# Optimization experiments

Hardware: AMD Instinct MI355X
Metric: run time of the kernel (lower is better)

## Reference

```python
import jax, jax.numpy as jnp
import numpy as np

B, T, HID = 2, 2048, 2048
NKH, NVH = 16, 32
DK, DV = 128, 128
R = NVH // NKH            # GQA repeat factor = 2
KDIM, VDIM = NKH * DK, NVH * DV   # 2048, 4096
CONV_K = 4
EPS = 1e-6


def _silu(x):
    return x * jax.nn.sigmoid(x)


def _l2norm(x, eps=1e-6):
    return x * jax.lax.rsqrt(jnp.sum(x * x, axis=-1, keepdims=True) + eps)


def setup_inputs() -> dict:
    key = jax.random.key(0)
    ks = jax.random.split(key, 8)
    w = lambda k, shape, sc=0.02: jax.random.normal(k, shape, jnp.float32) * sc
    return {
        "hidden_states": jax.random.normal(ks[0], (B, T, HID), jnp.float32),
        "W_qkvz": w(ks[1], (HID, 2 * KDIM + 2 * VDIM)),
        "W_ba": w(ks[2], (HID, 2 * NVH)),
        "conv_w": w(ks[3], (2 * KDIM + VDIM, CONV_K), 0.1),
        "dt_bias": jnp.ones((NVH,), jnp.float32),
        "A_log": jax.random.normal(ks[4], (NVH,), jnp.float32),
        "norm_weight": jnp.ones((DV,), jnp.float32),
        "W_out": w(ks[5], (VDIM, HID)),
    }


def reference(hidden_states, W_qkvz, W_ba, conv_w, dt_bias, A_log, norm_weight, W_out):
    Bv, Tv = hidden_states.shape[:2]
    # input projections
    qkvz = hidden_states @ W_qkvz              # [B,T,2*KDIM+2*VDIM]
    ba = hidden_states @ W_ba                  # [B,T,2*NVH]
    # fix_query_key_value_ordering: per k-head layout [dk, dk, R*dv, R*dv]
    qkvz = qkvz.reshape(Bv, Tv, NKH, 2 * DK + 2 * R * DV)
    q, k, v, z = jnp.split(qkvz, [DK, 2 * DK, 2 * DK + R * DV], axis=3)
    v = v.reshape(Bv, Tv, NVH, DV)
    z = z.reshape(Bv, Tv, NVH, DV)
    ba = ba.reshape(Bv, Tv, NKH, 2 * R)
    b, a = jnp.split(ba, 2, axis=3)
    b = b.reshape(Bv, Tv, NVH)
    a = a.reshape(Bv, Tv, NVH)
    # causal depthwise short conv over time + silu
    mixed = jnp.concatenate(
        [q.reshape(Bv, Tv, KDIM), k.reshape(Bv, Tv, KDIM), v.reshape(Bv, Tv, VDIM)], axis=-1)
    xp = jnp.pad(mixed, ((0, 0), (CONV_K - 1, 0), (0, 0)))
    conv = sum(xp[:, j:j + Tv, :] * conv_w[:, j] for j in range(CONV_K))
    conv = _silu(conv)
    q, k, v = jnp.split(conv, [KDIM, 2 * KDIM], axis=-1)
    q = q.reshape(Bv, Tv, NKH, DK)
    k = k.reshape(Bv, Tv, NKH, DK)
    v = v.reshape(Bv, Tv, NVH, DV)
    # gates
    beta = jax.nn.sigmoid(b)                                   # [B,T,H]
    g = -jnp.exp(A_log) * jax.nn.softplus(a + dt_bias)         # [B,T,H] log-decay
    alpha = jnp.exp(g)
    # GQA expansion + fused qk l2norm + scale
    q = jnp.repeat(q, R, axis=2)
    k = jnp.repeat(k, R, axis=2)
    q = _l2norm(q) * (DK ** -0.5)
    k = _l2norm(k)
    # gated delta rule recurrence over time; state S: [B,H,dk,dv]
    def step(S, inp):
        q_t, k_t, v_t, a_t, b_t = inp
        S = S * a_t[..., None, None]
        err = jnp.einsum('bhkv,bhk->bhv', S, k_t)
        v_new = (v_t - err) * b_t[..., None]
        S = S + k_t[..., None] * v_new[..., None, :]
        o = jnp.einsum('bhkv,bhk->bhv', S, q_t)
        return S, o

    tm = lambda x: jnp.swapaxes(x, 0, 1)  # time-major
    S0 = jnp.zeros((Bv, NVH, DK, DV), hidden_states.dtype)
    _, o = jax.lax.scan(step, S0, (tm(q), tm(k), tm(v), tm(alpha), tm(beta)))
    o = jnp.swapaxes(o, 0, 1)             # [B,T,H,DV]
    # gated RMSNorm (Mamba2 style: gate before norm)
    og = o * _silu(z)
    og = og * jax.lax.rsqrt(jnp.mean(og * og, axis=-1, keepdims=True) + EPS) * norm_weight
    return og.reshape(Bv, Tv, VDIM) @ W_out
```

## Files before the change

kernel.cpp:

```cpp
#include <hip/hip_runtime.h>
#include <hip/hip_bf16.h>

typedef __hip_bfloat16 bf16;
typedef __bf16 bf16x8_t __attribute__((ext_vector_type(8)));
typedef float f32x4 __attribute__((ext_vector_type(4)));
typedef unsigned short u16;

#define TB 2
#define TT 2048
#define THID 2048
#define TNKH 16
#define TNVH 32
#define TDK 128
#define TDV 128
#define TKDIM 2048
#define TVDIM 4096
#define CCH 64
#define NCH 32

__device__ __forceinline__ unsigned short f2bu(float f) {
  __hip_bfloat16 h = __float2bfloat16(f);
  return *reinterpret_cast<unsigned short*>(&h);
}
__device__ __forceinline__ float bu2f(unsigned short u) {
  __hip_bfloat16 h;
  *reinterpret_cast<unsigned short*>(&h) = u;
  return __bfloat162float(h);
}

__device__ __forceinline__ void gl_lds16(const bf16* g, u16* l) {
  __builtin_amdgcn_global_load_lds(
      (const __attribute__((address_space(1))) unsigned int*)g,
      (__attribute__((address_space(3))) unsigned int*)l, 16, 0, 0);
}

__global__ __launch_bounds__(256) void init_small_kernel(
    const void* __restrict__ dtb_raw, const void* __restrict__ alog_raw,
    const void* __restrict__ nw_raw,
    bf16* __restrict__ dtb_b, bf16* __restrict__ alog_b, bf16* __restrict__ nw_b,
    unsigned* __restrict__ flag)
{
  const unsigned* du = (const unsigned*)dtb_raw;
  const bool isb = (du[0] == 0x3F803F80u);
  const int t = threadIdx.x;
  if (t == 0) flag[0] = isb ? 1u : 0u;
  if (isb) {
    if (t < 32)       ((u16*)dtb_b)[t]       = ((const u16*)dtb_raw)[t];
    else if (t < 64)  ((u16*)alog_b)[t - 32] = ((const u16*)alog_raw)[t - 32];
    else if (t < 192) ((u16*)nw_b)[t - 64]   = ((const u16*)nw_raw)[t - 64];
  } else {
    if (t < 32)       dtb_b[t]        = __float2bfloat16(((const float*)dtb_raw)[t]);
    else if (t < 64)  alog_b[t - 32]  = __float2bfloat16(((const float*)alog_raw)[t - 32]);
    else if (t < 192) nw_b[t - 64]    = __float2bfloat16(((const float*)nw_raw)[t - 64]);
  }
}

__global__ __launch_bounds__(256) void convert_kernel(
    const void* __restrict__ src, bf16* __restrict__ dst, int n,
    const unsigned* __restrict__ dtb, int skipb) {
  const bool isb = (dtb[0] == 0x3F803F80u);
  if (isb && skipb) return;
  int i = blockIdx.x * 256 + threadIdx.x;
  const int stride = gridDim.x * 256;
  if (isb) {
    const unsigned short* s = (const unsigned short*)src;
    unsigned short* d = (unsigned short*)dst;
    for (; i < n; i += stride) d[i] = s[i];
  } else {
    const float* s = (const float*)src;
    for (; i < n; i += stride) dst[i] = __float2bfloat16(s[i]);
  }
}

__global__ __launch_bounds__(256) void transpose_convert_kernel(
    const void* __restrict__ src, bf16* __restrict__ dst, int K, int N,
    const unsigned* __restrict__ dtb) {
  __shared__ unsigned short tile[32][33];
  const bool isb = (dtb[0] == 0x3F803F80u);
  const int n0 = blockIdx.x * 32, k0 = blockIdx.y * 32;
  const int tx = threadIdx.x & 31, ty = threadIdx.x >> 5;
#pragma unroll
  for (int i = 0; i < 4; i++) {
    const int k = k0 + ty + i * 8;
    unsigned short v;
    if (isb) v = ((const unsigned short*)src)[(size_t)k * N + n0 + tx];
    else     v = f2bu(((const float*)src)[(size_t)k * N + n0 + tx]);
    tile[ty + i * 8][tx] = v;
  }
  __syncthreads();
#pragma unroll
  for (int i = 0; i < 4; i++) {
    const int n = n0 + ty + i * 8;
    ((unsigned short*)dst)[(size_t)n * K + k0 + tx] = tile[tx][ty + i * 8];
  }
}

#define PH_PRE()  do {                                                        \
    asm volatile("s_waitcnt lgkmcnt(0)" ::: "memory");                        \
    __builtin_amdgcn_sched_barrier(0); } while (0)
#define PH_POST() do { __builtin_amdgcn_sched_barrier(0);                     \
    __builtin_amdgcn_s_barrier(); } while (0)

#define STAGE_A(buf, kt, s)                                                   \
  gl_lds16(&Ak[(size_t)(m0 + (s) * 64 + srow) * lda + (kt) * 64 + scol],      \
           &lds[buf][0][((s) * 8192 + wave * 1024) >> 1])
#define STAGE_B(buf, kt, s)                                                   \
  gl_lds16(&Btk[(size_t)(n0 + (s) * 64 + srow) * ldb + (kt) * 64 + scol],     \
           &lds[buf][1][((s) * 8192 + wave * 1024) >> 1])

#define READ_A(buf, mh)                                                       \
  do {                                                                        \
    _Pragma("unroll")                                                         \
    for (int mi2 = 0; mi2 < 4; mi2++) {                                       \
      const int row_ = wm * 128 + (mh) * 64 + mi2 * 16 + l16;                 \
      aF[mi2][0] = *reinterpret_cast<const bf16x8_t*>(                        \
          &lds[buf][0][(row_ * 128 + koff0) >> 1]);                           \
      aF[mi2][1] = *reinterpret_cast<const bf16x8_t*>(                        \
          &lds[buf][0][(row_ * 128 + koff1) >> 1]);                           \
    }                                                                         \
  } while (0)

#define READ_B(buf, nh)                                                       \
  do {                                                                        \
    _Pragma("unroll")                                                         \
    for (int ni2 = 0; ni2 < 2; ni2++) {                                       \
      const int row_ = wn * 64 + ((nh) * 2 + ni2) * 16 + l16;                 \
      bF[(nh) * 2 + ni2][0] = *reinterpret_cast<const bf16x8_t*>(             \
          &lds[buf][1][(row_ * 128 + koff0) >> 1]);                           \
      bF[(nh) * 2 + ni2][1] = *reinterpret_cast<const bf16x8_t*>(             \
          &lds[buf][1][(row_ * 128 + koff1) >> 1]);                           \
    }                                                                         \
  } while (0)

#define MMA_Q(mh, nh)                                                         \
  do {                                                                        \
    __builtin_amdgcn_s_setprio(1);                                            \
    _Pragma("unroll")                                                         \
    for (int ks = 0; ks < 2; ks++)                                            \
      _Pragma("unroll")                                                       \
      for (int mi2 = 0; mi2 < 4; mi2++)                                       \
        _Pragma("unroll")                                                     \
        for (int ni2 = 0; ni2 < 2; ni2++)                                     \
          acc[(mh) * 4 + mi2][(nh) * 2 + ni2] =                               \
              __builtin_amdgcn_mfma_f32_16x16x32_bf16(                        \
                  aF[mi2][ks], bF[(nh) * 2 + ni2][ks],                        \
                  acc[(mh) * 4 + mi2][(nh) * 2 + ni2], 0, 0, 0);              \
    __builtin_amdgcn_s_setprio(0);                                            \
  } while (0)

template<int MODE>
__global__ __launch_bounds__(512, 2) void gemm256_kernel(
    const bf16* __restrict__ A, const bf16* __restrict__ Bt,
    void* __restrict__ C0, bf16* __restrict__ C1,
    int M, int N, int K, int lda, int ldb,
    const unsigned* __restrict__ flag, const void* __restrict__ Araw)
{
  __shared__ __align__(16) u16 lds[2][2][256 * 64];

  const int tid = threadIdx.x;
  const int wave = tid >> 6, lane = tid & 63;
  const int l16 = lane & 15, quad = lane >> 4;
  const int wm = wave >> 2, wn = wave & 3;

  const int nwg = gridDim.x * gridDim.y;
  const int lin = blockIdx.y * gridDim.x + blockIdx.x;
  const int cpx = nwg >> 3;
  const int sw = (lin & 7) * cpx + (lin >> 3);
  const int m0 = (sw / gridDim.x) * 256;
  const int n0 = (sw % gridDim.x) * 256;

  const bf16* Abase = A;
  if (MODE == 1 && Araw != nullptr && flag[0] != 0u)
    Abase = (const bf16*)Araw;

  const bf16* Ak  = Abase + (size_t)blockIdx.z * K;
  const bf16* Btk = Bt + (size_t)blockIdx.z * K;

  f32x4 acc[8][4];
#pragma unroll
  for (int i = 0; i < 8; i++)
#pragma unroll
    for (int j = 0; j < 4; j++) acc[i][j] = (f32x4){0.f, 0.f, 0.f, 0.f};

  const int o_lane = wave * 1024 + lane * 16;
  const int l_lane = o_lane ^ ((lane & 56) << 1);
  const int srow = l_lane >> 7;
  const int scol = (l_lane & 127) >> 1;
  const int koff0 = (quad * 16) ^ ((l16 & 7) << 4);
  const int koff1 = koff0 ^ 64;

  bf16x8_t aF[4][2], bF[4][2];

  const int NT = K >> 6;
  const int NIT = NT >> 1;

#pragma unroll
  for (int s = 0; s < 4; s++) STAGE_B(0, 0, s);
#pragma unroll
  for (int s = 0; s < 4; s++) STAGE_A(0, 0, s);
#pragma unroll
  for (int s = 0; s < 4; s++) STAGE_B(1, 1, s);
  asm volatile("s_waitcnt vmcnt(4)" ::: "memory");
  __builtin_amdgcn_s_barrier();

  for (int it = 0; it < NIT; ++it) {
    const int to = 2 * it + 1, te2 = 2 * it + 2, to2 = 2 * it + 3;
    const bool s2 = (te2 < NT), s3 = (to2 < NT);

    STAGE_A(1, to, 0); STAGE_A(1, to, 1);
    READ_A(0, 0); READ_B(0, 0);
    PH_PRE(); MMA_Q(0, 0); PH_POST();

    STAGE_A(1, to, 2); STAGE_A(1, to, 3);
    READ_B(0, 1);
    PH_PRE(); MMA_Q(0, 1); PH_POST();

    if (s2) { STAGE_B(0, te2, 0); STAGE_B(0, te2, 1); }
    READ_A(0, 1);
    PH_PRE(); MMA_Q(1, 1); PH_POST();

    if (s2) { STAGE_B(0, te2, 2); STAGE_B(0, te2, 3); }
    PH_PRE(); MMA_Q(1, 0);
    if (s2) asm volatile("s_waitcnt vmcnt(4)" ::: "memory");
    else    asm volatile("s_waitcnt vmcnt(0)" ::: "memory");
    PH_POST();

    if (s2) { STAGE_A(0, te2, 0); STAGE_A(0, te2, 1); }
    READ_A(1, 0); READ_B(1, 0);
    PH_PRE(); MMA_Q(0, 0); PH_POST();

    if (s2) { STAGE_A(0, te2, 2); STAGE_A(0, te2, 3); }
    READ_B(1, 1);
    PH_PRE(); MMA_Q(0, 1); PH_POST();

    if (s3) { STAGE_B(1, to2, 0); STAGE_B(1, to2, 1); }
    READ_A(1, 1);
    PH_PRE(); MMA_Q(1, 1); PH_POST();

    if (s3) { STAGE_B(1, to2, 2); STAGE_B(1, to2, 3); }
    PH_PRE(); MMA_Q(1, 0);
    if (s2) {
      if (s3) asm volatile("s_waitcnt vmcnt(4)" ::: "memory");
      else    asm volatile("s_waitcnt vmcnt(0)" ::: "memory");
    }
    PH_POST();
  }

#pragma unroll
  for (int mi = 0; mi < 8; mi++)
#pragma unroll
    for (int ni = 0; ni < 4; ni++)
#pragma unroll
      for (int r = 0; r < 4; r++) {
        const int row = m0 + wm * 128 + mi * 16 + quad * 4 + r;
        const int col = n0 + wn * 64 + ni * 16 + l16;
        const float fv = acc[mi][ni][r];
        if (MODE == 2) {
          float* Cp = (float*)C0 + (size_t)blockIdx.z * 4096 * 2048;
          Cp[(size_t)row * N + col] = fv;
        } else {
          const bf16 v = __float2bfloat16(fv);
          bf16* C0h = (bf16*)C0;
          const int hh = col / 768;
          const int idx = col - hh * 768;
          if (idx < 128) {
            C0h[(size_t)row * 8192 + hh * 128 + idx] = v;
          } else if (idx < 256) {
            C0h[(size_t)row * 8192 + 2048 + hh * 128 + (idx - 128)] = v;
          } else if (idx < 512) {
            const int u = idx - 256;
            C0h[(size_t)row * 8192 + 4096 + (hh * 2 + (u >> 7)) * 128 + (u & 127)] = v;
          } else {
            const int u = idx - 512;
            C1[(size_t)row * 4096 + (hh * 2 + (u >> 7)) * 128 + (u & 127)] = v;
          }
        }
      }
}

__global__ __launch_bounds__(256) void combine_kernel(
    const float* __restrict__ p, void* __restrict__ out,
    const unsigned* __restrict__ flag)
{
  const bool outbf = (flag[0] != 0u);
  const size_t i = ((size_t)blockIdx.x * 256 + threadIdx.x) * 4;
  const float4 a = *reinterpret_cast<const float4*>(&p[i]);
  const float4 b = *reinterpret_cast<const float4*>(&p[i + (size_t)4096 * 2048]);
  if (outbf) {
    unsigned short o[4];
    o[0] = f2bu(a.x + b.x); o[1] = f2bu(a.y + b.y);
    o[2] = f2bu(a.z + b.z); o[3] = f2bu(a.w + b.w);
    *reinterpret_cast<uint2*>((unsigned short*)out + i) =
        *reinterpret_cast<const uint2*>(o);
  } else {
    float4 s;
    s.x = a.x + b.x; s.y = a.y + b.y; s.z = a.z + b.z; s.w = a.w + b.w;
    *reinterpret_cast<float4*>((float*)out + i) = s;
  }
}

__global__ __launch_bounds__(256) void ba_gates_kernel(
    const bf16* __restrict__ hs, const void* __restrict__ hs_raw,
    const bf16* __restrict__ W_ba,
    const bf16* __restrict__ dt_bias, const bf16* __restrict__ A_log,
    float* __restrict__ gb, float* __restrict__ beta,
    const unsigned* __restrict__ flag)
{
  const int m = blockIdx.x * 4 + (threadIdx.x >> 6);
  const int c = threadIdx.x & 63;
  const bf16* hbase = (flag[0] != 0u) ? (const bf16*)hs_raw : hs;
  const bf16* hrow = hbase + (size_t)m * THID;
  float acc = 0.f;
  for (int k = 0; k < THID; k += 8) {
    const uint4 hv = *reinterpret_cast<const uint4*>(&hrow[k]);
    const unsigned short* hp = (const unsigned short*)&hv;
#pragma unroll
    for (int j = 0; j < 8; j++)
      acc += bu2f(hp[j]) * __bfloat162float(W_ba[(size_t)(k + j) * 64 + c]);
  }
  const int h = c >> 2, q = c & 3;
  if (q < 2) {
    beta[(size_t)m * TNVH + h * 2 + q] = 1.f / (1.f + __expf(-acc));
  } else {
    const int vh = h * 2 + (q - 2);
    const float av = acc + __bfloat162float(dt_bias[vh]);
    const float sp = (av > 20.f) ? av : log1pf(__expf(av));
    gb[(size_t)m * TNVH + vh] = -__expf(__bfloat162float(A_log[vh])) * sp;
  }
}

#define CTM 8
__global__ __launch_bounds__(128) void conv_kernel(
    const bf16* __restrict__ mixed, const bf16* __restrict__ conv_w,
    bf16* __restrict__ qn, bf16* __restrict__ kn, bf16* __restrict__ vc)
{
  __shared__ float red[CTM][2];
  const int g = blockIdx.x;
  const int m0 = blockIdx.y * CTM;
  const int tloc = m0 & (TT - 1);
  const int tid = threadIdx.x;
  const int c = g * 128 + tid;

  float w[4];
#pragma unroll
  for (int j = 0; j < 4; j++) w[j] = __bfloat162float(conv_w[c * 4 + j]);

  float xv[CTM + 3];
#pragma unroll
  for (int jj = 0; jj < CTM + 3; jj++) {
    const int row = m0 - 3 + jj;
    xv[jj] = (row >= 0) ? bu2f(((const unsigned short*)mixed)[(size_t)row * 8192 + c]) : 0.f;
  }

  float val[CTM];
#pragma unroll
  for (int u = 0; u < CTM; u++) {
    float s = 0.f;
#pragma unroll
    for (int j = 0; j < 4; j++) {
      if (tloc + u - 3 + j >= 0) s += xv[u + j] * w[j];
    }
    val[u] = s / (1.f + __expf(-s));
  }

  if (g < 32) {
#pragma unroll
    for (int u = 0; u < CTM; u++) {
      float s2 = val[u] * val[u];
#pragma unroll
      for (int off = 32; off; off >>= 1) s2 += __shfl_xor(s2, off);
      if ((tid & 63) == 0) red[u][tid >> 6] = s2;
    }
    __syncthreads();
#pragma unroll
    for (int u = 0; u < CTM; u++) {
      float scale = rsqrtf(red[u][0] + red[u][1] + 1e-6f);
      const int m = m0 + u;
      if (g < 16) {
        scale *= 0.08838834764831845f;
        qn[(size_t)m * TKDIM + g * 128 + tid] = __float2bfloat16(val[u] * scale);
      } else {
        kn[(size_t)m * TKDIM + (g - 16) * 128 + tid] = __float2bfloat16(val[u] * scale);
      }
    }
  } else {
#pragma unroll
    for (int u = 0; u < CTM; u++)
      vc[(size_t)(m0 + u) * TVDIM + (g - 32) * 128 + tid] = __float2bfloat16(val[u]);
  }
}

__global__ __launch_bounds__(256) void chunk_prep_kernel(
    const bf16* __restrict__ qn, const bf16* __restrict__ kn,
    const bf16* __restrict__ vc, const float* __restrict__ gb,
    const float* __restrict__ betab,
    bf16* __restrict__ Wbuf, bf16* __restrict__ U0buf,
    bf16* __restrict__ Pbuf, bf16* __restrict__ Ktt,
    float* __restrict__ egcbuf)
{
  __shared__ __align__(16) unsigned short Kb[64][136];
  __shared__ __align__(16) unsigned short Vb[64][136];
  __shared__ __align__(8) float Ms[64][66];
  __shared__ float gcl[64], bl[64], egl[64], ecl[64];

  const int cg = blockIdx.x;
  const int vh = blockIdx.y;
  const int h = vh >> 1;
  const int ch = cg * 32 + vh;
  const int m0 = cg * 64;
  const int tid = threadIdx.x;
  const int lane = tid & 63;
  const int w = tid >> 6, l16 = lane & 15, quad = lane >> 4;

  {
    const int row = tid >> 2, cb = (tid & 3) * 32;
#pragma unroll
    for (int u = 0; u < 4; u++) {
      *reinterpret_cast<uint4*>(&Kb[row][cb + u * 8]) =
          *reinterpret_cast<const uint4*>(&kn[(size_t)(m0 + row) * TKDIM + h * 128 + cb + u * 8]);
      *reinterpret_cast<uint4*>(&Vb[row][cb + u * 8]) =
          *reinterpret_cast<const uint4*>(&vc[(size_t)(m0 + row) * TVDIM + vh * 128 + cb + u * 8]);
    }
  }
  if (tid < 64) {
    float x = gb[(size_t)(m0 + tid) * TNVH + vh];
#pragma unroll
    for (int off = 1; off < 64; off <<= 1) {
      float y = __shfl_up(x, off);
      if (lane >= off) x += y;
    }
    gcl[tid] = x;
    egl[tid] = __expf(x);
    bl[tid] = betab[(size_t)(m0 + tid) * TNVH + vh];
  }
  __syncthreads();

  if (tid < 64) {
    ecl[tid] = __expf(gcl[63] - gcl[tid]);
    egcbuf[(size_t)ch * 64 + tid] = egl[tid];
  }

  f32x4 aKK[4], aQK[4];
#pragma unroll
  for (int i = 0; i < 4; i++) { aKK[i] = (f32x4){0.f,0.f,0.f,0.f}; aQK[i] = (f32x4){0.f,0.f,0.f,0.f}; }
#pragma unroll
  for (int kk = 0; kk < 4; kk++) {
    bf16x8_t kf = *reinterpret_cast<const bf16x8_t*>(&Kb[w * 16 + l16][kk * 32 + quad * 8]);
    bf16x8_t qf = *reinterpret_cast<const bf16x8_t*>(
        &qn[(size_t)(m0 + w * 16 + l16) * TKDIM + h * 128 + kk * 32 + quad * 8]);
#pragma unroll
    for (int nt = 0; nt < 4; nt++) {
      bf16x8_t bf = *reinterpret_cast<const bf16x8_t*>(&Kb[nt * 16 + l16][kk * 32 + quad * 8]);
      aKK[nt] = __builtin_amdgcn_mfma_f32_16x16x32_bf16(kf, bf, aKK[nt], 0, 0, 0);
      aQK[nt] = __builtin_amdgcn_mfma_f32_16x16x32_bf16(qf, bf, aQK[nt], 0, 0, 0);
    }
  }
#pragma unroll
  for (int nt = 0; nt < 4; nt++)
#pragma unroll
    for (int r = 0; r < 4; r++) {
      const int i = w * 16 + quad * 4 + r;
      const int s = nt * 16 + l16;
      const float d = gcl[i] - gcl[s];
      const float e = __expf(d);
      Ms[i][s] = (s < i) ? bl[i] * e * aKK[nt][r] : 0.f;
      const float pv = (s <= i) ? e * aQK[nt][r] : 0.f;
      Pbuf[(size_t)ch * 4096 + i * 64 + s] = __float2bfloat16(pv);
    }
  __syncthreads();

  {
    const int j = tid;
    float x[64];
    if (j < 128) {
#pragma unroll
      for (int i = 0; i < 64; i++) x[i] = bl[i] * egl[i] * bu2f(Kb[i][j]);
    } else {
#pragma unroll
      for (int i = 0; i < 64; i++) x[i] = bl[i] * bu2f(Vb[i][j - 128]);
    }
#pragma unroll
    for (int i = 1; i < 64; i++) {
      float xi = x[i];
#pragma unroll
      for (int s = 0; s < (i & ~1); s += 2) {
        const float2 m2 = *reinterpret_cast<const float2*>(&Ms[i][s]);
        xi -= m2.x * x[s] + m2.y * x[s + 1];
      }
      if (i & 1) xi -= Ms[i][i - 1] * x[i - 1];
      x[i] = xi;
    }
    if (j < 128) {
#pragma unroll
      for (int i = 0; i < 64; i++)
        Wbuf[(size_t)ch * 8192 + i * 128 + j] = __float2bfloat16(x[i]);
    } else {
#pragma unroll
      for (int i = 0; i < 64; i++)
        U0buf[(size_t)ch * 8192 + i * 128 + (j - 128)] = __float2bfloat16(x[i]);
    }
  }

#pragma unroll
  for (int u = 0; u < 32; u++) {
    const int idx = tid + u * 256;
    const int s = idx & 63, k = idx >> 6;
    Ktt[(size_t)ch * 8192 + k * 64 + s] = __float2bfloat16(bu2f(Kb[s][k]) * ecl[s]);
  }
}

__global__ __launch_bounds__(256) void chunk_scan_kernel(
    const bf16* __restrict__ qn, const bf16* __restrict__ zb,
    const float* __restrict__ egcbuf,
    const bf16* __restrict__ Wbuf, const bf16* __restrict__ U0buf,
    const bf16* __restrict__ Pbuf, const bf16* __restrict__ Ktt,
    bf16* __restrict__ ogbuf, float* __restrict__ psum)
{
  __shared__ __align__(16) unsigned short STb[32][136];
  __shared__ __align__(16) unsigned short uT[32][72];

  const int d = blockIdx.x;
  const int jj = d >> 3;
  const int bvh = (d & 7) * 8 + (jj >> 2);
  const int sl = jj & 3;
  const int b = bvh >> 5, vh = bvh & 31, h = vh >> 1;

  const int tid = threadIdx.x;
  const int w = tid >> 6, lane = tid & 63;
  const int l16 = lane & 15, quad = lane >> 4;
  const int vt = w & 1, kh = (w >> 1) * 64;

  for (int idx = tid; idx < 32 * 136; idx += 256) ((unsigned short*)STb)[idx] = 0;

  bf16x8_t wf[4], qf[4];
  unsigned short u0r[2][4];
  {
    const int ch0 = (b * 32) * 32 + vh;
    const int m00 = (b * 32) * 64;
#pragma unroll
    for (int kk = 0; kk < 4; kk++) {
      wf[kk] = *reinterpret_cast<const bf16x8_t*>(
          &Wbuf[(size_t)ch0 * 8192 + (w * 16 + l16) * 128 + kk * 32 + quad * 8]);
      qf[kk] = *reinterpret_cast<const bf16x8_t*>(
          &qn[(size_t)(m00 + w * 16 + l16) * TKDIM + h * 128 + kk * 32 + quad * 8]);
    }
#pragma unroll
    for (int nt = 0; nt < 2; nt++)
#pragma unroll
      for (int r = 0; r < 4; r++) {
        const int i = w * 16 + quad * 4 + r;
        const int dvg = sl * 32 + nt * 16 + l16;
        u0r[nt][r] = ((const unsigned short*)U0buf)[(size_t)ch0 * 8192 + i * 128 + dvg];
      }
  }
  f32x4 STreg[4];
#pragma unroll
  for (int i = 0; i < 4; i++) STreg[i] = (f32x4){0.f, 0.f, 0.f, 0.f};

  asm volatile("s_waitcnt lgkmcnt(0)" ::: "memory");
  __builtin_amdgcn_sched_barrier(0);
  __builtin_amdgcn_s_barrier();

  for (int c = 0; c < NCH; c++) {
    const int ch = (b * 32 + c) * 32 + vh;
    const int m0 = (b * 32 + c) * 64;
    const int cn = (c + 1 < NCH) ? c + 1 : c;
    const int chn = (b * 32 + cn) * 32 + vh;
    const int m0n = (b * 32 + cn) * 64;

    bf16x8_t wfn[4], qfn[4];
#pragma unroll
    for (int kk = 0; kk < 4; kk++) {
      wfn[kk] = *reinterpret_cast<const bf16x8_t*>(
          &Wbuf[(size_t)chn * 8192 + (w * 16 + l16) * 128 + kk * 32 + quad * 8]);
      qfn[kk] = *reinterpret_cast<const bf16x8_t*>(
          &qn[(size_t)(m0n + w * 16 + l16) * TKDIM + h * 128 + kk * 32 + quad * 8]);
    }
    unsigned short u0rn[2][4], zr[2][4];
#pragma unroll
    for (int nt = 0; nt < 2; nt++)
#pragma unroll
      for (int r = 0; r < 4; r++) {
        const int i = w * 16 + quad * 4 + r;
        const int dvg = sl * 32 + nt * 16 + l16;
        u0rn[nt][r] = ((const unsigned short*)U0buf)[(size_t)chn * 8192 + i * 128 + dvg];
        zr[nt][r]  = ((const unsigned short*)zb)[(size_t)(m0 + i) * TVDIM + vh * 128 + dvg];
      }
    bf16x8_t pf[2];
#pragma unroll
    for (int kk = 0; kk < 2; kk++)
      pf[kk] = *reinterpret_cast<const bf16x8_t*>(
          &Pbuf[(size_t)ch * 4096 + (w * 16 + l16) * 64 + kk * 32 + quad * 8]);
    bf16x8_t kttf[4][2];
#pragma unroll
    for (int nt = 0; nt < 4; nt++)
#pragma unroll
      for (int kk = 0; kk < 2; kk++)
        kttf[nt][kk] = *reinterpret_cast<const bf16x8_t*>(
            &Ktt[(size_t)ch * 8192 + (kh + nt * 16 + l16) * 64 + kk * 32 + quad * 8]);
    float egr[4];
#pragma unroll
    for (int r = 0; r < 4; r++)
      egr[r] = egcbuf[(size_t)ch * 64 + w * 16 + quad * 4 + r];
    const float egC = egcbuf[(size_t)ch * 64 + 63];

    f32x4 au[2], aq[2];
#pragma unroll
    for (int i = 0; i < 2; i++) { au[i] = (f32x4){0.f,0.f,0.f,0.f}; aq[i] = (f32x4){0.f,0.f,0.f,0.f}; }
#pragma unroll
    for (int kk = 0; kk < 4; kk++)
#pragma unroll
      for (int nt = 0; nt < 2; nt++) {
        bf16x8_t bfr = *reinterpret_cast<const bf16x8_t*>(
            &STb[nt * 16 + l16][kk * 32 + quad * 8]);
        au[nt] = __builtin_amdgcn_mfma_f32_16x16x32_bf16(wf[kk], bfr, au[nt], 0, 0, 0);
        aq[nt] = __builtin_amdgcn_mfma_f32_16x16x32_bf16(qf[kk], bfr, aq[nt], 0, 0, 0);
      }
#pragma unroll
    for (int nt = 0; nt < 2; nt++)
#pragma unroll
      for (int r = 0; r < 4; r++) {
        const int i = w * 16 + quad * 4 + r;
        uT[nt * 16 + l16][i] = f2bu(bu2f(u0r[nt][r]) - au[nt][r]);
      }
    asm volatile("s_waitcnt lgkmcnt(0)" ::: "memory");
    __builtin_amdgcn_sched_barrier(0);
    __builtin_amdgcn_s_barrier();

    f32x4 ao[2];
#pragma unroll
    for (int i = 0; i < 2; i++) ao[i] = (f32x4){0.f,0.f,0.f,0.f};
#pragma unroll
    for (int kk = 0; kk < 2; kk++)
#pragma unroll
      for (int nt = 0; nt < 2; nt++) {
        bf16x8_t bfr = *reinterpret_cast<const bf16x8_t*>(
            &uT[nt * 16 + l16][kk * 32 + quad * 8]);
        ao[nt] = __builtin_amdgcn_mfma_f32_16x16x32_bf16(pf[kk], bfr, ao[nt], 0, 0, 0);
      }
    float og[2][4];
#pragma unroll
    for (int nt = 0; nt < 2; nt++)
#pragma unroll
      for (int r = 0; r < 4; r++) {
        const float o = egr[r] * aq[nt][r] + ao[nt][r];
        const float zv = bu2f(zr[nt][r]);
        og[nt][r] = o * (zv / (1.f + __expf(-zv)));
      }
#pragma unroll
    for (int r = 0; r < 4; r++) {
      float ss = og[0][r] * og[0][r] + og[1][r] * og[1][r];
      ss += __shfl_xor(ss, 1); ss += __shfl_xor(ss, 2);
      ss += __shfl_xor(ss, 4); ss += __shfl_xor(ss, 8);
      if (l16 == 0)
        psum[(size_t)(m0 + w * 16 + quad * 4 + r) * 128 + vh * 4 + sl] = ss;
    }
#pragma unroll
    for (int nt = 0; nt < 2; nt++)
#pragma unroll
      for (int r = 0; r < 4; r++) {
        const int i = w * 16 + quad * 4 + r;
        const int dvg = sl * 32 + nt * 16 + l16;
        ((unsigned short*)ogbuf)[(size_t)(m0 + i) * TVDIM + vh * 128 + dvg] =
            f2bu(og[nt][r]);
      }

    bf16x8_t uf[2];
#pragma unroll
    for (int kk = 0; kk < 2; kk++)
      uf[kk] = *reinterpret_cast<const bf16x8_t*>(&uT[vt * 16 + l16][kk * 32 + quad * 8]);
    f32x4 as_[4];
#pragma unroll
    for (int i = 0; i < 4; i++) as_[i] = (f32x4){0.f,0.f,0.f,0.f};
#pragma unroll
    for (int nt = 0; nt < 4; nt++)
#pragma unroll
      for (int kk = 0; kk < 2; kk++)
        as_[nt] = __builtin_amdgcn_mfma_f32_16x16x32_bf16(uf[kk], kttf[nt][kk], as_[nt], 0, 0, 0);
#pragma unroll
    for (int nt = 0; nt < 4; nt++)
#pragma unroll
      for (int r = 0; r < 4; r++) {
        const float ns = egC * STreg[nt][r] + as_[nt][r];
        STreg[nt][r] = ns;
        STb[vt * 16 + quad * 4 + r][kh + nt * 16 + l16] = f2bu(ns);
      }

#pragma unroll
    for (int kk = 0; kk < 4; kk++) { wf[kk] = wfn[kk]; qf[kk] = qfn[kk]; }
#pragma unroll
    for (int nt = 0; nt < 2; nt++)
#pragma unroll
      for (int r = 0; r < 4; r++) u0r[nt][r] = u0rn[nt][r];
    asm volatile("s_waitcnt lgkmcnt(0)" ::: "memory");
    __builtin_amdgcn_sched_barrier(0);
    __builtin_amdgcn_s_barrier();
  }
}

__global__ __launch_bounds__(256) void norm_finish_kernel(
    bf16* __restrict__ og, const float* __restrict__ psum,
    const bf16* __restrict__ nw)
{
  const size_t idx = ((size_t)blockIdx.x * 256 + threadIdx.x) * 8;
  const int m = (int)(idx >> 12);
  const int col = (int)(idx & 4095);
  const int vh = col >> 7, dv = col & 127;
  const float* ps = &psum[(size_t)m * 128 + vh * 4];
  const float ms = (ps[0] + ps[1] + ps[2] + ps[3]) * (1.f / 128.f);
  const float sc = rsqrtf(ms + 1e-6f);
  uint4 v = *reinterpret_cast<const uint4*>(&og[idx]);
  uint4 wv = *reinterpret_cast<const uint4*>(&nw[dv]);
  unsigned short* vp = (unsigned short*)&v;
  unsigned short* wp = (unsigned short*)&wv;
  uint4 o;
  unsigned short* op = (unsigned short*)&o;
#pragma unroll
  for (int j = 0; j < 8; j++)
    op[j] = f2bu(bu2f(vp[j]) * sc * bu2f(wp[j]));
  *reinterpret_cast<uint4*>(&og[idx]) = o;
}

extern "C" void kernel_launch(void* const* d_in, const int* in_sizes, int n_in,
                              void* d_out, int out_size, void* d_ws, size_t ws_size,
                              hipStream_t stream) {
  const void* hs_raw   = d_in[0];
  const void* Wq_raw   = d_in[1];
  const void* Wba_raw  = d_in[2];
  const void* cw_raw   = d_in[3];
  const void* dtb_raw  = d_in[4];
  const void* Alog_raw = d_in[5];
  const void* nw_raw   = d_in[6];
  const void* Wout_raw = d_in[7];

  const size_t M = (size_t)TB * TT;
  char* p = (char*)d_ws;
  auto alloc = [&](size_t bytes) { char* r = p; p += (bytes + 255) & ~(size_t)255; return r; };
  unsigned* flag  = (unsigned*)alloc(256);
  bf16* hs_b   = (bf16*)alloc(M * THID * 2);
  bf16* WqT    = (bf16*)alloc((size_t)12288 * THID * 2);
  bf16* Wba_b  = (bf16*)alloc((size_t)THID * 64 * 2);
  bf16* cw_b   = (bf16*)alloc(8192 * 4 * 2);
  bf16* dtb_b  = (bf16*)alloc(64);
  bf16* Alog_b = (bf16*)alloc(64);
  bf16* nw_b   = (bf16*)alloc(256);
  bf16* WoutT  = (bf16*)alloc((size_t)THID * TVDIM * 2);
  bf16*  mixed  = (bf16*) alloc(M * 8192 * 2);
  bf16*  zbuf   = (bf16*) alloc(M * 4096 * 2);
  bf16*  qn     = (bf16*) alloc(M * 2048 * 2);
  bf16*  kn     = (bf16*) alloc(M * 2048 * 2);
  bf16*  vc     = (bf16*) alloc(M * 4096 * 2);
  float* gbuf   = (float*)alloc(M * 32 * 4);
  float* betab  = (float*)alloc(M * 32 * 4);
  float* egcbuf = (float*)alloc((size_t)2048 * 64 * 4);
  float* psum   = (float*)alloc(M * 128 * 4);

  bf16* Wbuf  = WqT;
  bf16* Pbuf  = WqT + (size_t)2048 * 64 * 128;
  bf16* U0buf = mixed;
  bf16* Ktt   = mixed + (size_t)2048 * 64 * 128;
  bf16* ogbuf = vc;
  float* part = (float*)mixed;

  const unsigned* dtb_u = (const unsigned*)dtb_raw;

  init_small_kernel<<<1, 256, 0, stream>>>(
      dtb_raw, Alog_raw, nw_raw, dtb_b, Alog_b, nw_b, flag);
  convert_kernel<<<2048, 256, 0, stream>>>(hs_raw, hs_b, (int)(M * THID), dtb_u, 1);
  transpose_convert_kernel<<<dim3(12288 / 32, 2048 / 32), 256, 0, stream>>>(
      Wq_raw, WqT, 2048, 12288, dtb_u);
  convert_kernel<<<128, 256, 0, stream>>>(Wba_raw, Wba_b, THID * 64, dtb_u, 0);
  convert_kernel<<<32,  256, 0, stream>>>(cw_raw,  cw_b,  8192 * 4,  dtb_u, 0);
  transpose_convert_kernel<<<dim3(2048 / 32, 4096 / 32), 256, 0, stream>>>(
      Wout_raw, WoutT, 4096, 2048, dtb_u);

  gemm256_kernel<1><<<dim3(12288 / 256, 4096 / 256), 512, 0, stream>>>(
      hs_b, WqT, mixed, zbuf, 4096, 12288, 2048, 2048, 2048, flag, hs_raw);
  ba_gates_kernel<<<4096 / 4, 256, 0, stream>>>(
      hs_b, hs_raw, Wba_b, dtb_b, Alog_b, gbuf, betab, flag);
  conv_kernel<<<dim3(64, 4096 / CTM), 128, 0, stream>>>(mixed, cw_b, qn, kn, vc);

  chunk_prep_kernel<<<dim3(64, 32), 256, 0, stream>>>(
      qn, kn, vc, gbuf, betab, Wbuf, U0buf, Pbuf, Ktt, egcbuf);
  chunk_scan_kernel<<<256, 256, 0, stream>>>(
      qn, zbuf, egcbuf, Wbuf, U0buf, Pbuf, Ktt, ogbuf, psum);
  norm_finish_kernel<<<8192, 256, 0, stream>>>(ogbuf, psum, nw_b);

  gemm256_kernel<2><<<dim3(2048 / 256, 4096 / 256, 2), 512, 0, stream>>>(
      ogbuf, WoutT, part, nullptr, 4096, 2048, 2048, 4096, 4096, flag, nullptr);
  combine_kernel<<<8192, 256, 0, stream>>>(part, d_out, flag);
}
```

Baseline: 864.2 us.

## Replace split-K output GEMM with 256x128 tile GEMM writing output directly

The output projection used to run as a split-K GEMM with two K halves, writing fp32 partials that a separate combine kernel summed and converted. It now runs as one full-K GEMM templated on a narrower 128-column N tile, so the grid still has 256 workgroups and the result, bf16 or fp32, is stored straight into the output. This drops the partial-buffer traffic and the extra combine launch, at the cost of a longer K loop per workgroup and a smaller B tile. Separately, the hidden-state convert kernel is launched with fewer blocks.

New measurement: 882.6 us. +2.1%, slower.

```diff
diff --git a/kernel.cpp b/kernel.cpp
--- a/kernel.cpp
+++ b/kernel.cpp
@@ -103,10 +103,10 @@
 
 #define STAGE_A(buf, kt, s)                                                   \
   gl_lds16(&Ak[(size_t)(m0 + (s) * 64 + srow) * lda + (kt) * 64 + scol],      \
-           &lds[buf][0][((s) * 8192 + wave * 1024) >> 1])
+           &lds[buf][((s) * 8192 + wave * 1024) >> 1])
 #define STAGE_B(buf, kt, s)                                                   \
   gl_lds16(&Btk[(size_t)(n0 + (s) * 64 + srow) * ldb + (kt) * 64 + scol],     \
-           &lds[buf][1][((s) * 8192 + wave * 1024) >> 1])
+           &lds[buf][16384 + (((s) * 8192 + wave * 1024) >> 1)])
 
 #define READ_A(buf, mh)                                                       \
   do {                                                                        \
@@ -114,21 +114,21 @@
     for (int mi2 = 0; mi2 < 4; mi2++) {                                       \
       const int row_ = wm * 128 + (mh) * 64 + mi2 * 16 + l16;                 \
       aF[mi2][0] = *reinterpret_cast<const bf16x8_t*>(                        \
-          &lds[buf][0][(row_ * 128 + koff0) >> 1]);                           \
+          &lds[buf][(row_ * 128 + koff0) >> 1]);                              \
       aF[mi2][1] = *reinterpret_cast<const bf16x8_t*>(                        \
-          &lds[buf][0][(row_ * 128 + koff1) >> 1]);                           \
+          &lds[buf][(row_ * 128 + koff1) >> 1]);                              \
     }                                                                         \
   } while (0)
 
 #define READ_B(buf, nh)                                                       \
   do {                                                                        \
     _Pragma("unroll")                                                         \
-    for (int ni2 = 0; ni2 < 2; ni2++) {                                       \
-      const int row_ = wn * 64 + ((nh) * 2 + ni2) * 16 + l16;                 \
-      bF[(nh) * 2 + ni2][0] = *reinterpret_cast<const bf16x8_t*>(             \
-          &lds[buf][1][(row_ * 128 + koff0) >> 1]);                           \
-      bF[(nh) * 2 + ni2][1] = *reinterpret_cast<const bf16x8_t*>(             \
-          &lds[buf][1][(row_ * 128 + koff1) >> 1]);                           \
+    for (int ni2 = 0; ni2 < NH; ni2++) {                                      \
+      const int row_ = wn * (NF * 16) + ((nh) * NH + ni2) * 16 + l16;         \
+      bF[(nh) * NH + ni2][0] = *reinterpret_cast<const bf16x8_t*>(            \
+          &lds[buf][16384 + ((row_ * 128 + koff0) >> 1)]);                    \
+      bF[(nh) * NH + ni2][1] = *reinterpret_cast<const bf16x8_t*>(            \
+          &lds[buf][16384 + ((row_ * 128 + koff1) >> 1)]);                    \
     }                                                                         \
   } while (0)
 
@@ -140,22 +140,30 @@
       _Pragma("unroll")                                                       \
       for (int mi2 = 0; mi2 < 4; mi2++)                                       \
         _Pragma("unroll")                                                     \
-        for (int ni2 = 0; ni2 < 2; ni2++)                                     \
-          acc[(mh) * 4 + mi2][(nh) * 2 + ni2] =                               \
+        for (int ni2 = 0; ni2 < NH; ni2++)                                    \
+          acc[(mh) * 4 + mi2][(nh) * NH + ni2] =                              \
               __builtin_amdgcn_mfma_f32_16x16x32_bf16(                        \
-                  aF[mi2][ks], bF[(nh) * 2 + ni2][ks],                        \
-                  acc[(mh) * 4 + mi2][(nh) * 2 + ni2], 0, 0, 0);              \
+                  aF[mi2][ks], bF[(nh) * NH + ni2][ks],                       \
+                  acc[(mh) * 4 + mi2][(nh) * NH + ni2], 0, 0, 0);             \
     __builtin_amdgcn_s_setprio(0);                                            \
   } while (0)
 
-template<int MODE>
+#define WAIT_NB() do {                                                        \
+    if (BN == 256) asm volatile("s_waitcnt vmcnt(4)" ::: "memory");           \
+    else           asm volatile("s_waitcnt vmcnt(2)" ::: "memory");           \
+  } while (0)
+
+template<int MODE, int BN>
 __global__ __launch_bounds__(512, 2) void gemm256_kernel(
     const bf16* __restrict__ A, const bf16* __restrict__ Bt,
     void* __restrict__ C0, bf16* __restrict__ C1,
     int M, int N, int K, int lda, int ldb,
     const unsigned* __restrict__ flag, const void* __restrict__ Araw)
 {
-  __shared__ __align__(16) u16 lds[2][2][256 * 64];
+  constexpr int NF = BN >> 6;
+  constexpr int NH = NF >> 1;
+  constexpr int NB = NF;
+  __shared__ __align__(16) u16 lds[2][(256 + BN) * 64];
 
   const int tid = threadIdx.x;
   const int wave = tid >> 6, lane = tid & 63;
@@ -167,20 +175,23 @@
   const int cpx = nwg >> 3;
   const int sw = (lin & 7) * cpx + (lin >> 3);
   const int m0 = (sw / gridDim.x) * 256;
-  const int n0 = (sw % gridDim.x) * 256;
+  const int n0 = (sw % gridDim.x) * BN;
 
   const bf16* Abase = A;
   if (MODE == 1 && Araw != nullptr && flag[0] != 0u)
     Abase = (const bf16*)Araw;
 
-  const bf16* Ak  = Abase + (size_t)blockIdx.z * K;
-  const bf16* Btk = Bt + (size_t)blockIdx.z * K;
-
-  f32x4 acc[8][4];
+  const bf16* Ak  = Abase;
+  const bf16* Btk = Bt;
+
+  bool outbf = false;
+  if (MODE == 0) outbf = (flag[0] != 0u);
+
+  f32x4 acc[8][NF];
 #pragma unroll
   for (int i = 0; i < 8; i++)
 #pragma unroll
-    for (int j = 0; j < 4; j++) acc[i][j] = (f32x4){0.f, 0.f, 0.f, 0.f};
+    for (int j = 0; j < NF; j++) acc[i][j] = (f32x4){0.f, 0.f, 0.f, 0.f};
 
   const int o_lane = wave * 1024 + lane * 16;
   const int l_lane = o_lane ^ ((lane & 56) << 1);
@@ -189,18 +200,18 @@
   const int koff0 = (quad * 16) ^ ((l16 & 7) << 4);
   const int koff1 = koff0 ^ 64;
 
-  bf16x8_t aF[4][2], bF[4][2];
+  bf16x8_t aF[4][2], bF[NF][2];
 
   const int NT = K >> 6;
   const int NIT = NT >> 1;
 
 #pragma unroll
-  for (int s = 0; s < 4; s++) STAGE_B(0, 0, s);
+  for (int s = 0; s < NB; s++) STAGE_B(0, 0, s);
 #pragma unroll
   for (int s = 0; s < 4; s++) STAGE_A(0, 0, s);
 #pragma unroll
-  for (int s = 0; s < 4; s++) STAGE_B(1, 1, s);
-  asm volatile("s_waitcnt vmcnt(4)" ::: "memory");
+  for (int s = 0; s < NB; s++) STAGE_B(1, 1, s);
+  WAIT_NB();
   __builtin_amdgcn_s_barrier();
 
   for (int it = 0; it < NIT; ++it) {
@@ -215,13 +226,19 @@
     READ_B(0, 1);
     PH_PRE(); MMA_Q(0, 1); PH_POST();
 
-    if (s2) { STAGE_B(0, te2, 0); STAGE_B(0, te2, 1); }
+    if (s2) {
+#pragma unroll
+      for (int s = 0; s < NB / 2; s++) STAGE_B(0, te2, s);
+    }
     READ_A(0, 1);
     PH_PRE(); MMA_Q(1, 1); PH_POST();
 
-    if (s2) { STAGE_B(0, te2, 2); STAGE_B(0, te2, 3); }
+    if (s2) {
+#pragma unroll
+      for (int s = NB / 2; s < NB; s++) STAGE_B(0, te2, s);
+    }
     PH_PRE(); MMA_Q(1, 0);
-    if (s2) asm volatile("s_waitcnt vmcnt(4)" ::: "memory");
+    if (s2) WAIT_NB();
     else    asm volatile("s_waitcnt vmcnt(0)" ::: "memory");
     PH_POST();
 
@@ -233,14 +250,20 @@
     READ_B(1, 1);
     PH_PRE(); MMA_Q(0, 1); PH_POST();
 
-    if (s3) { STAGE_B(1, to2, 0); STAGE_B(1, to2, 1); }
+    if (s3) {
+#pragma unroll
+      for (int s = 0; s < NB / 2; s++) STAGE_B(1, to2, s);
+    }
     READ_A(1, 1);
     PH_PRE(); MMA_Q(1, 1); PH_POST();
 
-    if (s3) { STAGE_B(1, to2, 2); STAGE_B(1, to2, 3); }
+    if (s3) {
+#pragma unroll
+      for (int s = NB / 2; s < NB; s++) STAGE_B(1, to2, s);
+    }
     PH_PRE(); MMA_Q(1, 0);
     if (s2) {
-      if (s3) asm volatile("s_waitcnt vmcnt(4)" ::: "memory");
+      if (s3) WAIT_NB();
       else    asm volatile("s_waitcnt vmcnt(0)" ::: "memory");
     }
     PH_POST();
@@ -249,15 +272,15 @@
 #pragma unroll
   for (int mi = 0; mi < 8; mi++)
 #pragma unroll
-    for (int ni = 0; ni < 4; ni++)
+    for (int ni = 0; ni < NF; ni++)
 #pragma unroll
       for (int r = 0; r < 4; r++) {
         const int row = m0 + wm * 128 + mi * 16 + quad * 4 + r;
-        const int col = n0 + wn * 64 + ni * 16 + l16;
+        const int col = n0 + wn * (NF * 16) + ni * 16 + l16;
         const float fv = acc[mi][ni][r];
-        if (MODE == 2) {
-          float* Cp = (float*)C0 + (size_t)blockIdx.z * 4096 * 2048;
-          Cp[(size_t)row * N + col] = fv;
+        if (MODE == 0) {
+          if (outbf) ((bf16*)C0)[(size_t)row * N + col] = __float2bfloat16(fv);
+          else       ((float*)C0)[(size_t)row * N + col] = fv;
         } else {
           const bf16 v = __float2bfloat16(fv);
           bf16* C0h = (bf16*)C0;
@@ -276,27 +299,6 @@
           }
         }
       }
-}
-
-__global__ __launch_bounds__(256) void combine_kernel(
-    const float* __restrict__ p, void* __restrict__ out,
-    const unsigned* __restrict__ flag)
-{
-  const bool outbf = (flag[0] != 0u);
-  const size_t i = ((size_t)blockIdx.x * 256 + threadIdx.x) * 4;
-  const float4 a = *reinterpret_cast<const float4*>(&p[i]);
-  const float4 b = *reinterpret_cast<const float4*>(&p[i + (size_t)4096 * 2048]);
-  if (outbf) {
-    unsigned short o[4];
-    o[0] = f2bu(a.x + b.x); o[1] = f2bu(a.y + b.y);
-    o[2] = f2bu(a.z + b.z); o[3] = f2bu(a.w + b.w);
-    *reinterpret_cast<uint2*>((unsigned short*)out + i) =
-        *reinterpret_cast<const uint2*>(o);
-  } else {
-    float4 s;
-    s.x = a.x + b.x; s.y = a.y + b.y; s.z = a.z + b.z; s.w = a.w + b.w;
-    *reinterpret_cast<float4*>((float*)out + i) = s;
-  }
 }
 
 __global__ __launch_bounds__(256) void ba_gates_kernel(
@@ -760,13 +762,12 @@
   bf16* U0buf = mixed;
   bf16* Ktt   = mixed + (size_t)2048 * 64 * 128;
   bf16* ogbuf = vc;
-  float* part = (float*)mixed;
 
   const unsigned* dtb_u = (const unsigned*)dtb_raw;
 
   init_small_kernel<<<1, 256, 0, stream>>>(
       dtb_raw, Alog_raw, nw_raw, dtb_b, Alog_b, nw_b, flag);
-  convert_kernel<<<2048, 256, 0, stream>>>(hs_raw, hs_b, (int)(M * THID), dtb_u, 1);
+  convert_kernel<<<256, 256, 0, stream>>>(hs_raw, hs_b, (int)(M * THID), dtb_u, 1);
   transpose_convert_kernel<<<dim3(12288 / 32, 2048 / 32), 256, 0, stream>>>(
       Wq_raw, WqT, 2048, 12288, dtb_u);
   convert_kernel<<<128, 256, 0, stream>>>(Wba_raw, Wba_b, THID * 64, dtb_u, 0);
@@ -774,7 +775,7 @@
   transpose_convert_kernel<<<dim3(2048 / 32, 4096 / 32), 256, 0, stream>>>(
       Wout_raw, WoutT, 4096, 2048, dtb_u);
 
-  gemm256_kernel<1><<<dim3(12288 / 256, 4096 / 256), 512, 0, stream>>>(
+  gemm256_kernel<1, 256><<<dim3(12288 / 256, 4096 / 256), 512, 0, stream>>>(
       hs_b, WqT, mixed, zbuf, 4096, 12288, 2048, 2048, 2048, flag, hs_raw);
   ba_gates_kernel<<<4096 / 4, 256, 0, stream>>>(
       hs_b, hs_raw, Wba_b, dtb_b, Alog_b, gbuf, betab, flag);
@@ -786,7 +787,6 @@
       qn, zbuf, egcbuf, Wbuf, U0buf, Pbuf, Ktt, ogbuf, psum);
   norm_finish_kernel<<<8192, 256, 0, stream>>>(ogbuf, psum, nw_b);
 
-  gemm256_kernel<2><<<dim3(2048 / 256, 4096 / 256, 2), 512, 0, stream>>>(
-      ogbuf, WoutT, part, nullptr, 4096, 2048, 2048, 4096, 4096, flag, nullptr);
-  combine_kernel<<<8192, 256, 0, stream>>>(part, d_out, flag);
-}
+  gemm256_kernel<0, 128><<<dim3(2048 / 128, 4096 / 256), 512, 0, stream>>>(
+      ogbuf, WoutT, d_out, nullptr, 4096, 2048, 4096, 4096, 4096, flag, nullptr);
+}
```
